# Kernel optimization log

Measured on AMD Instinct MI355X. Metric: run time of the kernel, lower is better.

## Reference

```python
import math
import jax, jax.numpy as jnp
from jax import lax
import numpy as np

B, T, D = 4, 8192, 1024
NUM_PATCHES = 512
EPS = 1e-6

def setup_inputs() -> dict:
    key = jax.random.key(0)
    ks = jax.random.split(key, 4)
    h = D // 2
    x = jax.random.normal(ks[0], (B, T, D), dtype=jnp.float32)
    conv1_w = jax.random.normal(ks[1], (h, D, 3), dtype=jnp.float32) * 0.02
    conv1_b = jnp.zeros((h,), jnp.float32)
    conv2_w = jax.random.normal(ks[2], (1, h, 3), dtype=jnp.float32) * 0.02
    conv2_b = jnp.zeros((1,), jnp.float32)
    norm_w = jnp.ones((D,), jnp.float32)
    return {"x": x, "conv1_w": conv1_w, "conv1_b": conv1_b,
            "conv2_w": conv2_w, "conv2_b": conv2_b, "norm_w": norm_w}

def _conv1d(x_ncw, w, b):
    y = lax.conv_general_dilated(x_ncw, w, window_strides=(1,), padding=[(1, 1)],
                                 dimension_numbers=("NCW", "OIW", "NCW"))
    return y + b[None, :, None]

def reference(x, conv1_w, conv1_b, conv2_w, conv2_b, norm_w):
    b, t, d = x.shape
    k = NUM_PATCHES
    seg = t // k  # T divisible by k, so all segments have equal length

    # LearnedBoundaryPredictor: conv -> gelu -> conv -> logits (B, T)
    xc = jnp.transpose(x, (0, 2, 1))  # (B, D, T)
    hcv = jax.nn.gelu(_conv1d(xc, conv1_w, conv1_b), approximate=False)
    logits = _conv1d(hcv, conv2_w, conv2_b)[:, 0, :]  # (B, T)

    # per-segment softmax-weighted centroid + normalized entropy (vectorized)
    seg_logits = logits.reshape(b, k, seg)
    w = jax.nn.softmax(seg_logits, axis=-1)                      # (B, k, seg)
    pos = jnp.arange(t, dtype=x.dtype).reshape(1, k, seg)
    boundaries = jnp.sum(w * pos, axis=-1)                        # (B, k)
    ent = -jnp.sum(w * jnp.log(jnp.clip(w, 1e-8)), axis=-1)
    entropy_signal = ent / jnp.asarray(math.log(max(seg, 2)), x.dtype)

    # gather byte embeddings at integer boundary positions
    idx = jnp.clip(boundaries.astype(jnp.int32), 0, t - 1)       # (B, k)
    patches = jnp.take_along_axis(x, idx[:, :, None], axis=1)    # (B, k, D)

    # RMSNorm
    rms = lax.rsqrt(jnp.mean(patches * patches, axis=-1, keepdims=True) + EPS)
    out = patches * rms * norm_w
    return out, entropy_signal
```

## Files before the change

### kernel.cpp

```cpp
#include <hip/hip_runtime.h>
#include <hip/hip_bf16.h>
#include <math.h>

#define T_LEN 8192
#define D_DIM 1024
#define H_DIM 512
#define NPATCH 512
#define SEG 16

typedef _Float16 f16;
typedef _Float16 f16x4 __attribute__((ext_vector_type(4)));
typedef _Float16 f16x8 __attribute__((ext_vector_type(8)));
typedef float f32x4 __attribute__((ext_vector_type(4)));

#define BMR 256
#define BNR 128
#define NBM2 128
#define NBN2 4
#define QL2 258
#define PADT (T_LEN + 2)
#define RSCALE 2048.0f
#define RINV   4.8828125e-4f

__device__ __forceinline__ void gll16(const void* g, void* l) {
    __builtin_amdgcn_global_load_lds((const __attribute__((address_space(1))) void*)g,
                                     (__attribute__((address_space(3))) void*)l, 16, 0, 0);
}

__global__ __launch_bounds__(256) void k_split_x(const float* __restrict__ x,
                                                 f16* __restrict__ xh, f16* __restrict__ xls) {
    size_t i4 = (size_t)blockIdx.x * 256 + threadIdx.x;
    size_t e = i4 * 4;
    int d = (int)(e % D_DIM);
    size_t row = e / D_DIM;
    int pt = (int)(row % PADT);
    int b = (int)(row / PADT);
    f16x4 h, lo;
    if (pt == 0 || pt == PADT - 1) {
        h = (f16x4){0, 0, 0, 0}; lo = (f16x4){0, 0, 0, 0};
    } else {
        float4 v = *(const float4*)(x + ((size_t)b * T_LEN + pt - 1) * D_DIM + d);
        f16 h0 = (f16)v.x, h1 = (f16)v.y, h2 = (f16)v.z, h3 = (f16)v.w;
        h = (f16x4){h0, h1, h2, h3};
        lo = (f16x4){(f16)((v.x - (float)h0) * RSCALE), (f16)((v.y - (float)h1) * RSCALE),
                     (f16)((v.z - (float)h2) * RSCALE), (f16)((v.w - (float)h3) * RSCALE)};
    }
    *(f16x4*)(xh + e) = h;
    *(f16x4*)(xls + e) = lo;
}

__global__ void k_split_w(const float* __restrict__ w1, f16* __restrict__ ws) {
    int idx = blockIdx.x * 256 + threadIdx.x;
    if (idx >= 3 * H_DIM * D_DIM) return;
    int i = idx % D_DIM;
    int o = (idx / D_DIM) % H_DIM;
    int j = idx / (D_DIM * H_DIM);
    float v = w1[((size_t)o * D_DIM + i) * 3 + j];
    f16 h = (f16)v;
    f16 l = (f16)((v - (float)h) * RSCALE);
    ws[((size_t)(j * 2 + 0) * H_DIM + o) * D_DIM + i] = h;
    ws[((size_t)(j * 2 + 1) * H_DIM + o) * D_DIM + i] = l;
}

__global__ __launch_bounds__(512, 2) void k_conv_gemm_f16(
    const f16* __restrict__ xh, const f16* __restrict__ xls,
    const f16* __restrict__ wsd, const float* __restrict__ b1,
    const float* __restrict__ w2, float* __restrict__ partials)
{
    __shared__ __align__(16) char smem[55296];
    const int tid = threadIdx.x;
    const int l = tid & 63, wv = tid >> 6;
    const int wr = wv >> 1, wc = wv & 1;

    int bid = blockIdx.x;
    int logical = (bid & 7) * 64 + (bid >> 3);
    const int bm = logical >> 2, bn = logical & 3;
    const int batch = bm >> 5;
    const int lt0 = (bm & 31) * BMR;
    const int n0 = bn * BNR;

    f32x4 ahh[4][4], axx[4][4];
    #pragma unroll
    for (int mi = 0; mi < 4; ++mi)
        #pragma unroll
        for (int nj = 0; nj < 4; ++nj) {
            ahh[mi][nj] = (f32x4){0.f, 0.f, 0.f, 0.f};
            axx[mi][nj] = (f32x4){0.f, 0.f, 0.f, 0.f};
        }

    const int kb = l >> 4, c15 = l & 15;

    for (int j = 0; j < 3; ++j) {
        const f16* ap[6];
        #pragma unroll
        for (int u = 0; u < 6; ++u) {
            int s = wv * 6 + u;
            if (s < 32) {
                int which = s >> 4, sl = s & 15;
                int m = sl * 16 + (l >> 2);
                int ch = (l & 3) ^ ((m >> 1) & 3);
                size_t base = ((size_t)batch * PADT + lt0 + j) * D_DIM;
                ap[u] = (which ? xls : xh) + base + (size_t)m * D_DIM + ch * 8;
            } else {
                int s2 = s - 32, which = s2 >> 3, sl = s2 & 7;
                int n = sl * 16 + (l >> 2);
                int ch = (l & 3) ^ ((n >> 1) & 3);
                size_t base = ((size_t)(j * 2 + which) * H_DIM + n0) * D_DIM;
                ap[u] = wsd + base + (size_t)n * D_DIM + ch * 8;
            }
        }
        for (int k0 = 0; k0 < D_DIM; k0 += 32) {
            #pragma unroll
            for (int u = 0; u < 6; ++u) {
                gll16(ap[u], smem + (wv * 6 + u) * 1024);
                ap[u] += 32;
            }
            __syncthreads();

            f16x8 bh[4], bl[4];
            #pragma unroll
            for (int nj = 0; nj < 4; ++nj) {
                int n = wc * 64 + nj * 16 + c15;
                int boff = n * 64 + ((kb ^ ((n >> 1) & 3)) * 16);
                bh[nj] = *(const f16x8*)(smem + 32768 + boff);
                bl[nj] = *(const f16x8*)(smem + 40960 + boff);
            }
            #pragma unroll
            for (int mi = 0; mi < 4; ++mi) {
                int m = wr * 64 + mi * 16 + c15;
                int aoff = m * 64 + ((kb ^ ((m >> 1) & 3)) * 16);
                f16x8 ah = *(const f16x8*)(smem + aoff);
                f16x8 al = *(const f16x8*)(smem + 16384 + aoff);
                #pragma unroll
                for (int nj = 0; nj < 4; ++nj) {
                    ahh[mi][nj] = __builtin_amdgcn_mfma_f32_16x16x32_f16(ah, bh[nj], ahh[mi][nj], 0, 0, 0);
                    axx[mi][nj] = __builtin_amdgcn_mfma_f32_16x16x32_f16(ah, bl[nj], axx[mi][nj], 0, 0, 0);
                    axx[mi][nj] = __builtin_amdgcn_mfma_f32_16x16x32_f16(al, bh[nj], axx[mi][nj], 0, 0, 0);
                }
            }
            __syncthreads();
        }
    }

    float* lp_lds = (float*)(smem + 49152);
    #pragma unroll
    for (int mi = 0; mi < 4; ++mi) {
        float lp[4][3] = {};
        #pragma unroll
        for (int nj = 0; nj < 4; ++nj) {
            int n = n0 + wc * 64 + nj * 16 + c15;
            float bias = b1[n];
            float w2m1 = w2[n * 3 + 2];
            float w20  = w2[n * 3 + 1];
            float w2p1 = w2[n * 3 + 0];
            #pragma unroll
            for (int r = 0; r < 4; ++r) {
                float v = ahh[mi][nj][r] + axx[mi][nj][r] * RINV + bias;
                float g = 0.5f * v * (1.f + erff(v * 0.70710678118654752f));
                lp[r][0] = fmaf(g, w2m1, lp[r][0]);
                lp[r][1] = fmaf(g, w20,  lp[r][1]);
                lp[r][2] = fmaf(g, w2p1, lp[r][2]);
            }
        }
        #pragma unroll
        for (int r = 0; r < 4; ++r)
            #pragma unroll
            for (int d = 0; d < 3; ++d) {
                float v = lp[r][d];
                v += __shfl_xor(v, 1, 64);
                v += __shfl_xor(v, 2, 64);
                v += __shfl_xor(v, 4, 64);
                v += __shfl_xor(v, 8, 64);
                lp[r][d] = v;
            }
        if (c15 == 0) {
            int m = wr * 64 + mi * 16 + kb * 4;
            #pragma unroll
            for (int r = 0; r < 4; ++r)
                #pragma unroll
                for (int d = 0; d < 3; ++d)
                    lp_lds[(wc * 3 + d) * 256 + m + r] = lp[r][d];
        }
    }
    __syncthreads();

    float* pout = partials + (size_t)(bm * NBN2 + bn) * QL2;
    for (int q = tid; q < QL2; q += 512) {
        int tloc = lt0 + q - 1;
        if (tloc >= 0 && tloc < T_LEN) {
            float v = 0.f;
            #pragma unroll
            for (int w2c = 0; w2c < 2; ++w2c) {
                if (q >= 1 && q <= 256) v += lp_lds[(w2c * 3 + 1) * 256 + q - 1];
                if (q >= 2)             v += lp_lds[(w2c * 3 + 2) * 256 + q - 2];
                if (q < 256)            v += lp_lds[(w2c * 3 + 0) * 256 + q];
            }
            pout[q] = v;
        }
    }
}

__global__ void k_reduce2(const float* __restrict__ partials,
                          const float* __restrict__ b2, float* __restrict__ logits) {
    int M = blockIdx.x * 256 + threadIdx.x;
    if (M >= 4 * T_LEN) return;
    int t = M & (T_LEN - 1);
    int bm = M >> 8;
    int mq = M & 255;
    int q = mq + 1;
    float s = b2[0];
    #pragma unroll
    for (int bn = 0; bn < NBN2; ++bn)
        s += partials[(size_t)(bm * NBN2 + bn) * QL2 + q];
    if (mq == 0 && t != 0) {
        #pragma unroll
        for (int bn = 0; bn < NBN2; ++bn)
            s += partials[(size_t)((bm - 1) * NBN2 + bn) * QL2 + (QL2 - 1)];
    }
    if (mq == 255 && t != T_LEN - 1) {
        #pragma unroll
        for (int bn = 0; bn < NBN2; ++bn)
            s += partials[(size_t)((bm + 1) * NBN2 + bn) * QL2 + 0];
    }
    logits[M] = s;
}

__global__ __launch_bounds__(256) void k_finalize(
    const float* __restrict__ x, const float* __restrict__ logits,
    const float* __restrict__ norm_w, float* __restrict__ out)
{
    int blk = blockIdx.x;
    int b = blk >> 9, p = blk & 511;
    const float* lg = logits + b * T_LEN + p * SEG;

    float l[SEG];
    #pragma unroll
    for (int i = 0; i < SEG; ++i) l[i] = lg[i];
    float mx = l[0];
    #pragma unroll
    for (int i = 1; i < SEG; ++i) mx = fmaxf(mx, l[i]);
    float w[SEG];
    float s = 0.f;
    #pragma unroll
    for (int i = 0; i < SEG; ++i) { w[i] = expf(l[i] - mx); s += w[i]; }
    float inv = 1.f / s;
    float boundary = 0.f, ent = 0.f;
    #pragma unroll
    for (int i = 0; i < SEG; ++i) {
        float wi = w[i] * inv;
        boundary += wi * (float)(p * SEG + i);
        ent -= wi * logf(fmaxf(wi, 1e-8f));
    }
    ent *= 0.36067376022224085f;

    int idx = (int)boundary;
    idx = min(max(idx, 0), T_LEN - 1);

    const float* row = x + ((size_t)b * T_LEN + idx) * D_DIM;
    int tid = threadIdx.x;
    float v[4];
    float ss = 0.f;
    #pragma unroll
    for (int r = 0; r < 4; ++r) {
        int c = tid + r * 256;
        v[r] = row[c];
        ss = fmaf(v[r], v[r], ss);
    }
    #pragma unroll
    for (int off = 32; off > 0; off >>= 1) ss += __shfl_down(ss, off, 64);
    __shared__ float sred[4];
    if ((tid & 63) == 0) sred[tid >> 6] = ss;
    __syncthreads();
    float tot = sred[0] + sred[1] + sred[2] + sred[3];
    float rms = rsqrtf(tot * (1.f / 1024.f) + 1e-6f);

    float* o0 = out + ((size_t)b * NPATCH + p) * D_DIM;
    #pragma unroll
    for (int r = 0; r < 4; ++r) {
        int c = tid + r * 256;
        o0[c] = v[r] * rms * norm_w[c];
    }
    if (tid == 0)
        out[(size_t)4 * NPATCH * D_DIM + b * NPATCH + p] = ent;
}

#define BM 128
#define BN 128
#define BK 16
#define NBM (4 * T_LEN / BM)
#define NBN (H_DIM / BN)
#define QLEN 130

__global__ void k_transpose_w1(const float* __restrict__ w1, float* __restrict__ w1t) {
    int idx = blockIdx.x * 256 + threadIdx.x;
    if (idx >= 3 * D_DIM * H_DIM) return;
    int o = idx % H_DIM;
    int i = (idx / H_DIM) % D_DIM;
    int j = idx / (H_DIM * D_DIM);
    w1t[idx] = w1[(o * D_DIM + i) * 3 + j];
}

__global__ __launch_bounds__(256) void k_conv_gemm(
    const float* __restrict__ x, const float* __restrict__ w1t,
    const float* __restrict__ b1, const float* __restrict__ w2,
    float* __restrict__ partials)
{
    __shared__ float As[BK][BM + 4];
    __shared__ float Bs[BK][BN];
    __shared__ float ld_lp[3][BM];

    const int bm = blockIdx.x, bn = blockIdx.y;
    const int m0 = bm * BM;
    const int batch = m0 / T_LEN;
    const int t0 = m0 % T_LEN;
    const int n0 = bn * BN;
    const int tid = threadIdx.x;
    const int tx = tid & 15, ty = tid >> 4;

    float acc[8][8] = {};

    const int a_col = (tid & 3) * 4;
    const int a_row = tid >> 2;
    const int b_row = tid >> 5;
    const int b_col = (tid & 31) * 4;

    const float* xb = x + (size_t)batch * T_LEN * D_DIM;

    for (int j = 0; j < 3; ++j) {
        const float* wj = w1t + (size_t)j * D_DIM * H_DIM;
        const int tshift = j - 1;
        for (int k0 = 0; k0 < D_DIM; k0 += BK) {
            #pragma unroll
            for (int rr = 0; rr < 2; ++rr) {
                int m = a_row + rr * 64;
                int tt = t0 + m + tshift;
                float4 v = make_float4(0.f, 0.f, 0.f, 0.f);
                if (tt >= 0 && tt < T_LEN)
                    v = *(const float4*)(xb + (size_t)tt * D_DIM + k0 + a_col);
                As[a_col + 0][m] = v.x; As[a_col + 1][m] = v.y;
                As[a_col + 2][m] = v.z; As[a_col + 3][m] = v.w;
            }
            #pragma unroll
            for (int rr = 0; rr < 2; ++rr) {
                int kk = b_row + rr * 8;
                *(float4*)&Bs[kk][b_col] =
                    *(const float4*)(wj + (size_t)(k0 + kk) * H_DIM + n0 + b_col);
            }
            __syncthreads();
            #pragma unroll
            for (int kk = 0; kk < BK; ++kk) {
                float a[8], bb[8];
                *(float4*)&a[0]  = *(const float4*)&As[kk][ty * 8];
                *(float4*)&a[4]  = *(const float4*)&As[kk][ty * 8 + 4];
                *(float4*)&bb[0] = *(const float4*)&Bs[kk][tx * 8];
                *(float4*)&bb[4] = *(const float4*)&Bs[kk][tx * 8 + 4];
                #pragma unroll
                for (int i = 0; i < 8; ++i) {
                    #pragma unroll
                    for (int ll = 0; ll < 8; ++ll)
                        acc[i][ll] = fmaf(a[i], bb[ll], acc[i][ll]);
                }
            }
            __syncthreads();
        }
    }

    float lp[8][3];
    #pragma unroll
    for (int i = 0; i < 8; ++i) { lp[i][0] = 0.f; lp[i][1] = 0.f; lp[i][2] = 0.f; }
    #pragma unroll
    for (int ll = 0; ll < 8; ++ll) {
        int n = n0 + tx * 8 + ll;
        float bias = b1[n];
        float w2m1 = w2[n * 3 + 2];
        float w20  = w2[n * 3 + 1];
        float w2p1 = w2[n * 3 + 0];
        #pragma unroll
        for (int i = 0; i < 8; ++i) {
            float v = acc[i][ll] + bias;
            float g = 0.5f * v * (1.f + erff(v * 0.70710678118654752f));
            lp[i][0] = fmaf(g, w2m1, lp[i][0]);
            lp[i][1] = fmaf(g, w20,  lp[i][1]);
            lp[i][2] = fmaf(g, w2p1, lp[i][2]);
        }
    }
    #pragma unroll
    for (int i = 0; i < 8; ++i) {
        #pragma unroll
        for (int d = 0; d < 3; ++d) {
            float v = lp[i][d];
            v += __shfl_xor(v, 1, 64);
            v += __shfl_xor(v, 2, 64);
            v += __shfl_xor(v, 4, 64);
            v += __shfl_xor(v, 8, 64);
            lp[i][d] = v;
        }
    }
    if (tx == 0) {
        #pragma unroll
        for (int i = 0; i < 8; ++i) {
            ld_lp[0][ty * 8 + i] = lp[i][0];
            ld_lp[1][ty * 8 + i] = lp[i][1];
            ld_lp[2][ty * 8 + i] = lp[i][2];
        }
    }
    __syncthreads();
    float* pout = partials + (size_t)(bm * NBN + bn) * QLEN;
    for (int q = tid; q < QLEN; q += 256) {
        int t = t0 + q - 1;
        if (t >= 0 && t < T_LEN) {
            float v = 0.f;
            if (q >= 1 && q <= BM) v += ld_lp[1][q - 1];
            if (q >= 2)            v += ld_lp[2][q - 2];
            if (q < BM)            v += ld_lp[0][q];
            pout[q] = v;
        }
    }
}

__global__ void k_reduce_logits(const float* __restrict__ partials,
                                const float* __restrict__ b2,
                                float* __restrict__ logits) {
    int M = blockIdx.x * 256 + threadIdx.x;
    if (M >= 4 * T_LEN) return;
    int t = M % T_LEN;
    int bm = M / BM;
    int q = (M % BM) + 1;
    float s = b2[0];
    #pragma unroll
    for (int bn = 0; bn < NBN; ++bn)
        s += partials[(size_t)(bm * NBN + bn) * QLEN + q];
    if ((M % BM) == 0 && t != 0) {
        #pragma unroll
        for (int bn = 0; bn < NBN; ++bn)
            s += partials[(size_t)((bm - 1) * NBN + bn) * QLEN + (QLEN - 1)];
    }
    if ((M % BM) == BM - 1 && t != T_LEN - 1) {
        #pragma unroll
        for (int bn = 0; bn < NBN; ++bn)
            s += partials[(size_t)((bm + 1) * NBN + bn) * QLEN + 0];
    }
    logits[M] = s;
}

extern "C" void kernel_launch(void* const* d_in, const int* in_sizes, int n_in,
                              void* d_out, int out_size, void* d_ws, size_t ws_size,
                              hipStream_t stream) {
    const float* x  = (const float*)d_in[0];
    const float* w1 = (const float*)d_in[1];
    const float* b1 = (const float*)d_in[2];
    const float* w2 = (const float*)d_in[3];
    const float* b2 = (const float*)d_in[4];
    const float* nw = (const float*)d_in[5];
    float* out = (float*)d_out;

    const size_t XS_ELEMS = (size_t)4 * PADT * D_DIM;
    const size_t WS_ELEMS = (size_t)3 * 2 * H_DIM * D_DIM;
    const size_t P2_FLOATS = (size_t)NBM2 * NBN2 * QL2;
    const size_t NEED = XS_ELEMS * 2 * sizeof(f16) + WS_ELEMS * sizeof(f16)
                      + (P2_FLOATS + 4 * T_LEN) * sizeof(float);

    if (ws_size >= NEED) {
        f16* xh = (f16*)d_ws;
        f16* xls = xh + XS_ELEMS;
        f16* wsd = xls + XS_ELEMS;
        float* partials = (float*)(wsd + WS_ELEMS);
        float* logits = partials + P2_FLOATS;

        k_split_x<<<(int)(XS_ELEMS / 4 / 256), 256, 0, stream>>>(x, xh, xls);
        k_split_w<<<(3 * H_DIM * D_DIM + 255) / 256, 256, 0, stream>>>(w1, wsd);
        k_conv_gemm_f16<<<NBM2 * NBN2, 512, 0, stream>>>(xh, xls, wsd, b1, w2, partials);
        k_reduce2<<<(4 * T_LEN + 255) / 256, 256, 0, stream>>>(partials, b2, logits);
        k_finalize<<<2048, 256, 0, stream>>>(x, logits, nw, out);
    } else {
        float* w1t      = (float*)d_ws;
        float* partials = w1t + 3 * D_DIM * H_DIM;
        float* logits   = partials + (size_t)NBM * NBN * QLEN;

        k_transpose_w1<<<(3 * D_DIM * H_DIM + 255) / 256, 256, 0, stream>>>(w1, w1t);
        k_conv_gemm<<<dim3(NBM, NBN), 256, 0, stream>>>(x, w1t, b1, w2, partials);
        k_reduce_logits<<<(4 * T_LEN + 255) / 256, 256, 0, stream>>>(partials, b2, logits);
        k_finalize<<<2048, 256, 0, stream>>>(x, logits, nw, out);
    }
}
```

Before: 405.6 us.

## Triple-buffer conv GEMM LDS staging with interleaved async loads and MFMA phases

Replaces the single-buffered, two-barrier k-loop in the conv GEMM with a flattened 96-step loop over a triple-buffered LDS ring, prefetching two steps ahead via global_load_lds. Loads for the next stages are issued in pairs between MFMA quadrants, and the MFMA blocks are wrapped in s_setprio to favour compute issue. The aim is to hide global-memory latency behind the MFMAs. In exchange, LDS use grows to about 150KB per block, which may cut the two blocks per CU that launch_bounds targets, and the loop adds more barriers.

```diff
diff --git a/kernel.cpp b/kernel.cpp
--- a/kernel.cpp
+++ b/kernel.cpp
@@ -21,6 +21,9 @@
 #define PADT (T_LEN + 2)
 #define RSCALE 2048.0f
 #define RINV   4.8828125e-4f
+
+#define BUFB 49152
+#define NSTEP 96
 
 __device__ __forceinline__ void gll16(const void* g, void* l) {
     __builtin_amdgcn_global_load_lds((const __attribute__((address_space(1))) void*)g,
@@ -62,12 +65,26 @@
     ws[((size_t)(j * 2 + 1) * H_DIM + o) * D_DIM + i] = l;
 }
 
+#define MM3(mi, nj, AH, AL, BH, BL)                                                       \
+    ahh[mi][nj] = __builtin_amdgcn_mfma_f32_16x16x32_f16(AH, BH, ahh[mi][nj], 0, 0, 0);   \
+    axx[mi][nj] = __builtin_amdgcn_mfma_f32_16x16x32_f16(AH, BL, axx[mi][nj], 0, 0, 0);   \
+    axx[mi][nj] = __builtin_amdgcn_mfma_f32_16x16x32_f16(AL, BH, axx[mi][nj], 0, 0, 0);
+
+#define STAGE_PAIR(SV, U0, U1)                                                            \
+    { int sv_ = (SV);                                                                     \
+      if (sv_ < NSTEP) {                                                                  \
+          char* dsty = smem + (sv_ % 3) * BUFB;                                           \
+          int jj_ = sv_ >> 5; int ko_ = (sv_ & 31) * 32;                                  \
+          gll16(base0[U0] + (size_t)jj_ * jstr[U0] + ko_, dsty + (wv * 6 + U0) * 1024);   \
+          gll16(base0[U1] + (size_t)jj_ * jstr[U1] + ko_, dsty + (wv * 6 + U1) * 1024);   \
+      } }
+
 __global__ __launch_bounds__(512, 2) void k_conv_gemm_f16(
     const f16* __restrict__ xh, const f16* __restrict__ xls,
     const f16* __restrict__ wsd, const float* __restrict__ b1,
     const float* __restrict__ w2, float* __restrict__ partials)
 {
-    __shared__ __align__(16) char smem[55296];
+    __shared__ __align__(16) char smem[3 * BUFB + 6144];
     const int tid = threadIdx.x;
     const int l = tid & 63, wv = tid >> 6;
     const int wr = wv >> 1, wc = wv & 1;
@@ -90,59 +107,97 @@
 
     const int kb = l >> 4, c15 = l & 15;
 
-    for (int j = 0; j < 3; ++j) {
-        const f16* ap[6];
-        #pragma unroll
-        for (int u = 0; u < 6; ++u) {
-            int s = wv * 6 + u;
-            if (s < 32) {
-                int which = s >> 4, sl = s & 15;
-                int m = sl * 16 + (l >> 2);
-                int ch = (l & 3) ^ ((m >> 1) & 3);
-                size_t base = ((size_t)batch * PADT + lt0 + j) * D_DIM;
-                ap[u] = (which ? xls : xh) + base + (size_t)m * D_DIM + ch * 8;
-            } else {
-                int s2 = s - 32, which = s2 >> 3, sl = s2 & 7;
-                int n = sl * 16 + (l >> 2);
-                int ch = (l & 3) ^ ((n >> 1) & 3);
-                size_t base = ((size_t)(j * 2 + which) * H_DIM + n0) * D_DIM;
-                ap[u] = wsd + base + (size_t)n * D_DIM + ch * 8;
-            }
-        }
-        for (int k0 = 0; k0 < D_DIM; k0 += 32) {
-            #pragma unroll
-            for (int u = 0; u < 6; ++u) {
-                gll16(ap[u], smem + (wv * 6 + u) * 1024);
-                ap[u] += 32;
-            }
-            __syncthreads();
-
-            f16x8 bh[4], bl[4];
-            #pragma unroll
-            for (int nj = 0; nj < 4; ++nj) {
-                int n = wc * 64 + nj * 16 + c15;
-                int boff = n * 64 + ((kb ^ ((n >> 1) & 3)) * 16);
-                bh[nj] = *(const f16x8*)(smem + 32768 + boff);
-                bl[nj] = *(const f16x8*)(smem + 40960 + boff);
-            }
-            #pragma unroll
-            for (int mi = 0; mi < 4; ++mi) {
-                int m = wr * 64 + mi * 16 + c15;
-                int aoff = m * 64 + ((kb ^ ((m >> 1) & 3)) * 16);
-                f16x8 ah = *(const f16x8*)(smem + aoff);
-                f16x8 al = *(const f16x8*)(smem + 16384 + aoff);
-                #pragma unroll
-                for (int nj = 0; nj < 4; ++nj) {
-                    ahh[mi][nj] = __builtin_amdgcn_mfma_f32_16x16x32_f16(ah, bh[nj], ahh[mi][nj], 0, 0, 0);
-                    axx[mi][nj] = __builtin_amdgcn_mfma_f32_16x16x32_f16(ah, bl[nj], axx[mi][nj], 0, 0, 0);
-                    axx[mi][nj] = __builtin_amdgcn_mfma_f32_16x16x32_f16(al, bh[nj], axx[mi][nj], 0, 0, 0);
-                }
-            }
-            __syncthreads();
-        }
-    }
-
-    float* lp_lds = (float*)(smem + 49152);
+    const f16* base0[6];
+    int jstr[6];
+    #pragma unroll
+    for (int u = 0; u < 6; ++u) {
+        int s = wv * 6 + u;
+        if (s < 32) {
+            int which = s >> 4, sl = s & 15;
+            int m = sl * 16 + (l >> 2);
+            int ch = (l & 3) ^ ((m >> 1) & 3);
+            base0[u] = (which ? xls : xh) + ((size_t)batch * PADT + lt0) * D_DIM
+                       + (size_t)m * D_DIM + ch * 8;
+            jstr[u] = D_DIM;
+        } else {
+            int s2 = s - 32, which = s2 >> 3, sl = s2 & 7;
+            int n = sl * 16 + (l >> 2);
+            int ch = (l & 3) ^ ((n >> 1) & 3);
+            base0[u] = wsd + ((size_t)which * H_DIM + n0) * D_DIM + (size_t)n * D_DIM + ch * 8;
+            jstr[u] = 2 * H_DIM * D_DIM;
+        }
+    }
+
+    int aoff_[4], boff_[4];
+    #pragma unroll
+    for (int mi = 0; mi < 4; ++mi) {
+        int m = wr * 64 + mi * 16 + c15;
+        aoff_[mi] = m * 64 + ((kb ^ ((m >> 1) & 3)) * 16);
+    }
+    #pragma unroll
+    for (int nj = 0; nj < 4; ++nj) {
+        int n = wc * 64 + nj * 16 + c15;
+        boff_[nj] = n * 64 + ((kb ^ ((n >> 1) & 3)) * 16);
+    }
+
+    #pragma unroll
+    for (int u = 0; u < 6; ++u)
+        gll16(base0[u], smem + (wv * 6 + u) * 1024);
+    #pragma unroll
+    for (int u = 0; u < 6; ++u)
+        gll16(base0[u] + 32, smem + BUFB + (wv * 6 + u) * 1024);
+    asm volatile("s_waitcnt vmcnt(6)" ::: "memory");
+    __builtin_amdgcn_s_barrier();
+
+    for (int t = 0; t < NSTEP; ++t) {
+        char* buf = smem + (t % 3) * BUFB;
+        f16x8 ah0, al0, ah1, al1, ah2, al2, ah3, al3;
+        f16x8 bh0, bl0, bh1, bl1, bh2, bl2, bh3, bl3;
+
+        ah0 = *(const f16x8*)(buf + aoff_[0]);          al0 = *(const f16x8*)(buf + 16384 + aoff_[0]);
+        ah1 = *(const f16x8*)(buf + aoff_[1]);          al1 = *(const f16x8*)(buf + 16384 + aoff_[1]);
+        bh0 = *(const f16x8*)(buf + 32768 + boff_[0]);  bl0 = *(const f16x8*)(buf + 40960 + boff_[0]);
+        bh1 = *(const f16x8*)(buf + 32768 + boff_[1]);  bl1 = *(const f16x8*)(buf + 40960 + boff_[1]);
+        STAGE_PAIR(t + 2, 0, 1);
+        __builtin_amdgcn_s_barrier();
+        __builtin_amdgcn_s_setprio(1);
+        MM3(0, 0, ah0, al0, bh0, bl0); MM3(0, 1, ah0, al0, bh1, bl1);
+        MM3(1, 0, ah1, al1, bh0, bl0); MM3(1, 1, ah1, al1, bh1, bl1);
+        __builtin_amdgcn_s_setprio(0);
+        __builtin_amdgcn_s_barrier();
+
+        ah2 = *(const f16x8*)(buf + aoff_[2]);          al2 = *(const f16x8*)(buf + 16384 + aoff_[2]);
+        ah3 = *(const f16x8*)(buf + aoff_[3]);          al3 = *(const f16x8*)(buf + 16384 + aoff_[3]);
+        STAGE_PAIR(t + 2, 2, 3);
+        __builtin_amdgcn_s_barrier();
+        __builtin_amdgcn_s_setprio(1);
+        MM3(2, 0, ah2, al2, bh0, bl0); MM3(2, 1, ah2, al2, bh1, bl1);
+        MM3(3, 0, ah3, al3, bh0, bl0); MM3(3, 1, ah3, al3, bh1, bl1);
+        __builtin_amdgcn_s_setprio(0);
+        __builtin_amdgcn_s_barrier();
+
+        bh2 = *(const f16x8*)(buf + 32768 + boff_[2]);  bl2 = *(const f16x8*)(buf + 40960 + boff_[2]);
+        bh3 = *(const f16x8*)(buf + 32768 + boff_[3]);  bl3 = *(const f16x8*)(buf + 40960 + boff_[3]);
+        STAGE_PAIR(t + 2, 4, 5);
+        __builtin_amdgcn_s_barrier();
+        __builtin_amdgcn_s_setprio(1);
+        MM3(2, 2, ah2, al2, bh2, bl2); MM3(2, 3, ah2, al2, bh3, bl3);
+        MM3(3, 2, ah3, al3, bh2, bl2); MM3(3, 3, ah3, al3, bh3, bl3);
+        __builtin_amdgcn_s_setprio(0);
+        __builtin_amdgcn_s_barrier();
+
+        __builtin_amdgcn_s_setprio(1);
+        MM3(0, 2, ah0, al0, bh2, bl2); MM3(0, 3, ah0, al0, bh3, bl3);
+        MM3(1, 2, ah1, al1, bh2, bl2); MM3(1, 3, ah1, al1, bh3, bl3);
+        __builtin_amdgcn_s_setprio(0);
+        if (t < NSTEP - 2)
+            asm volatile("s_waitcnt vmcnt(6)" ::: "memory");
+        else if (t == NSTEP - 2)
+            asm volatile("s_waitcnt vmcnt(0)" ::: "memory");
+        __builtin_amdgcn_s_barrier();
+    }
+
+    float* lp_lds = (float*)(smem + 3 * BUFB);
     #pragma unroll
     for (int mi = 0; mi < 4; ++mi) {
         float lp[4][3] = {};
```

Measured after the change: 357.1 us. 1.14x faster.

## Double-buffer LDS in conv GEMM with smaller 128x128 tiles and fused tap loop

Applied to the files above, without the earlier changes.

Rewrites the f16 split-precision conv GEMM to use 128x128 tiles with 256 threads and 1024 blocks. The three conv taps are merged into one 96-step K loop, and LDS is double-buffered so the next global-to-LDS load overlaps the current MFMAs, with one barrier per step and raised wave priority during the MFMAs. The old dedicated reduce kernel is dropped in favour of the existing k_reduce_logits with matching partial sizes. The cost is smaller tiles, which means more redundant A/B traffic per output, and the code depends on NBM/NBN/QLEN matching the new 128-row tiling.

```diff
diff --git a/kernel.cpp b/kernel.cpp
--- a/kernel.cpp
+++ b/kernel.cpp
@@ -13,14 +13,11 @@
 typedef _Float16 f16x8 __attribute__((ext_vector_type(8)));
 typedef float f32x4 __attribute__((ext_vector_type(4)));
 
-#define BMR 256
-#define BNR 128
-#define NBM2 128
-#define NBN2 4
-#define QL2 258
 #define PADT (T_LEN + 2)
 #define RSCALE 2048.0f
 #define RINV   4.8828125e-4f
+#define NSTEP 96
+#define BUF2B 32768
 
 __device__ __forceinline__ void gll16(const void* g, void* l) {
     __builtin_amdgcn_global_load_lds((const __attribute__((address_space(1))) void*)g,
@@ -62,22 +59,69 @@
     ws[((size_t)(j * 2 + 1) * H_DIM + o) * D_DIM + i] = l;
 }
 
-__global__ __launch_bounds__(512, 2) void k_conv_gemm_f16(
+#define MM3(mi, nj, AH, AL, BH, BL)                                                       \
+    ahh[mi][nj] = __builtin_amdgcn_mfma_f32_16x16x32_f16(AH, BH, ahh[mi][nj], 0, 0, 0);   \
+    axx[mi][nj] = __builtin_amdgcn_mfma_f32_16x16x32_f16(AH, BL, axx[mi][nj], 0, 0, 0);   \
+    axx[mi][nj] = __builtin_amdgcn_mfma_f32_16x16x32_f16(AL, BH, axx[mi][nj], 0, 0, 0);
+
+#define STEP(T_, RB_, DB_)                                                                \
+{                                                                                         \
+    const int t_ = (T_);                                                                  \
+    char* buf = (RB_);                                                                    \
+             \
+    if (t_ + 1 < NSTEP) {                                                                 \
+        char* dsty = (DB_);                                                               \
+        _Pragma("unroll")                                                                 \
+        for (int u = 0; u < 8; ++u)                                                       \
+            gll16(ap[u], dsty + (wv * 8 + u) * 1024);                                     \
+    }                                                                                     \
+    {                                                                                     \
+        bool bnd = (((t_ + 1) & 31) == 31);                                               \
+        _Pragma("unroll")                                                                 \
+        for (int u = 0; u < 8; ++u)                                                       \
+            ap[u] += bnd ? (jstr[u] - 992) : 32;                                          \
+    }                                                                                     \
+    f16x8 ah0, al0, ah1, al1, ah2, al2, ah3, al3;                                         \
+    f16x8 bh0, bl0, bh1, bl1, bh2, bl2, bh3, bl3;                                         \
+    ah0 = *(const f16x8*)(buf + aoff_[0]);          al0 = *(const f16x8*)(buf + 8192 + aoff_[0]);   \
+    ah1 = *(const f16x8*)(buf + aoff_[1]);          al1 = *(const f16x8*)(buf + 8192 + aoff_[1]);   \
+    ah2 = *(const f16x8*)(buf + aoff_[2]);          al2 = *(const f16x8*)(buf + 8192 + aoff_[2]);   \
+    ah3 = *(const f16x8*)(buf + aoff_[3]);          al3 = *(const f16x8*)(buf + 8192 + aoff_[3]);   \
+    bh0 = *(const f16x8*)(buf + 16384 + boff_[0]);  bl0 = *(const f16x8*)(buf + 24576 + boff_[0]);  \
+    bh1 = *(const f16x8*)(buf + 16384 + boff_[1]);  bl1 = *(const f16x8*)(buf + 24576 + boff_[1]);  \
+    bh2 = *(const f16x8*)(buf + 16384 + boff_[2]);  bl2 = *(const f16x8*)(buf + 24576 + boff_[2]);  \
+    bh3 = *(const f16x8*)(buf + 16384 + boff_[3]);  bl3 = *(const f16x8*)(buf + 24576 + boff_[3]);  \
+    __builtin_amdgcn_s_setprio(1);                                                        \
+    MM3(0, 0, ah0, al0, bh0, bl0); MM3(0, 1, ah0, al0, bh1, bl1);                         \
+    MM3(1, 0, ah1, al1, bh0, bl0); MM3(1, 1, ah1, al1, bh1, bl1);                         \
+    MM3(2, 0, ah2, al2, bh0, bl0); MM3(2, 1, ah2, al2, bh1, bl1);                         \
+    MM3(3, 0, ah3, al3, bh0, bl0); MM3(3, 1, ah3, al3, bh1, bl1);                         \
+    MM3(2, 2, ah2, al2, bh2, bl2); MM3(2, 3, ah2, al2, bh3, bl3);                         \
+    MM3(3, 2, ah3, al3, bh2, bl2); MM3(3, 3, ah3, al3, bh3, bl3);                         \
+    MM3(0, 2, ah0, al0, bh2, bl2); MM3(0, 3, ah0, al0, bh3, bl3);                         \
+    MM3(1, 2, ah1, al1, bh2, bl2); MM3(1, 3, ah1, al1, bh3, bl3);                         \
+    __builtin_amdgcn_s_setprio(0);                                                        \
+    if (t_ < NSTEP - 1)                                                                   \
+        asm volatile("s_waitcnt vmcnt(0)" ::: "memory");                                  \
+    __builtin_amdgcn_s_barrier();                                                         \
+}
+
+__global__ __launch_bounds__(256, 2) void k_conv_gemm_f16(
     const f16* __restrict__ xh, const f16* __restrict__ xls,
     const f16* __restrict__ wsd, const float* __restrict__ b1,
     const float* __restrict__ w2, float* __restrict__ partials)
 {
-    __shared__ __align__(16) char smem[55296];
+    __shared__ __align__(16) char smem[2 * BUF2B + 3072];
     const int tid = threadIdx.x;
     const int l = tid & 63, wv = tid >> 6;
     const int wr = wv >> 1, wc = wv & 1;
 
     int bid = blockIdx.x;
-    int logical = (bid & 7) * 64 + (bid >> 3);
+    int logical = (bid & 7) * 128 + (bid >> 3);
     const int bm = logical >> 2, bn = logical & 3;
-    const int batch = bm >> 5;
-    const int lt0 = (bm & 31) * BMR;
-    const int n0 = bn * BNR;
+    const int batch = bm >> 6;
+    const int lt0 = (bm & 63) * 128;
+    const int n0 = bn * 128;
 
     f32x4 ahh[4][4], axx[4][4];
     #pragma unroll
@@ -90,59 +134,55 @@
 
     const int kb = l >> 4, c15 = l & 15;
 
-    for (int j = 0; j < 3; ++j) {
-        const f16* ap[6];
-        #pragma unroll
-        for (int u = 0; u < 6; ++u) {
-            int s = wv * 6 + u;
-            if (s < 32) {
-                int which = s >> 4, sl = s & 15;
-                int m = sl * 16 + (l >> 2);
-                int ch = (l & 3) ^ ((m >> 1) & 3);
-                size_t base = ((size_t)batch * PADT + lt0 + j) * D_DIM;
-                ap[u] = (which ? xls : xh) + base + (size_t)m * D_DIM + ch * 8;
-            } else {
-                int s2 = s - 32, which = s2 >> 3, sl = s2 & 7;
-                int n = sl * 16 + (l >> 2);
-                int ch = (l & 3) ^ ((n >> 1) & 3);
-                size_t base = ((size_t)(j * 2 + which) * H_DIM + n0) * D_DIM;
-                ap[u] = wsd + base + (size_t)n * D_DIM + ch * 8;
-            }
-        }
-        for (int k0 = 0; k0 < D_DIM; k0 += 32) {
-            #pragma unroll
-            for (int u = 0; u < 6; ++u) {
-                gll16(ap[u], smem + (wv * 6 + u) * 1024);
-                ap[u] += 32;
-            }
-            __syncthreads();
-
-            f16x8 bh[4], bl[4];
-            #pragma unroll
-            for (int nj = 0; nj < 4; ++nj) {
-                int n = wc * 64 + nj * 16 + c15;
-                int boff = n * 64 + ((kb ^ ((n >> 1) & 3)) * 16);
-                bh[nj] = *(const f16x8*)(smem + 32768 + boff);
-                bl[nj] = *(const f16x8*)(smem + 40960 + boff);
-            }
-            #pragma unroll
-            for (int mi = 0; mi < 4; ++mi) {
-                int m = wr * 64 + mi * 16 + c15;
-                int aoff = m * 64 + ((kb ^ ((m >> 1) & 3)) * 16);
-                f16x8 ah = *(const f16x8*)(smem + aoff);
-                f16x8 al = *(const f16x8*)(smem + 16384 + aoff);
-                #pragma unroll
-                for (int nj = 0; nj < 4; ++nj) {
-                    ahh[mi][nj] = __builtin_amdgcn_mfma_f32_16x16x32_f16(ah, bh[nj], ahh[mi][nj], 0, 0, 0);
-                    axx[mi][nj] = __builtin_amdgcn_mfma_f32_16x16x32_f16(ah, bl[nj], axx[mi][nj], 0, 0, 0);
-                    axx[mi][nj] = __builtin_amdgcn_mfma_f32_16x16x32_f16(al, bh[nj], axx[mi][nj], 0, 0, 0);
-                }
-            }
-            __syncthreads();
-        }
-    }
-
-    float* lp_lds = (float*)(smem + 49152);
+    const f16* base0[8];
+    int jstr[8];
+    #pragma unroll
+    for (int u = 0; u < 8; ++u) {
+        int S = wv * 8 + u;
+        int sl = S & 7;
+        int m = sl * 16 + (l >> 2);
+        int ch = (l & 3) ^ ((m >> 1) & 3);
+        if (S < 16) {
+            const f16* src = (S < 8) ? xh : xls;
+            base0[u] = src + ((size_t)batch * PADT + lt0) * D_DIM + (size_t)m * D_DIM + ch * 8;
+            jstr[u] = D_DIM;
+        } else {
+            int which = (S >= 24);
+            base0[u] = wsd + ((size_t)which * H_DIM + n0) * D_DIM + (size_t)m * D_DIM + ch * 8;
+            jstr[u] = 2 * H_DIM * D_DIM;
+        }
+    }
+
+    int aoff_[4], boff_[4];
+    #pragma unroll
+    for (int mi = 0; mi < 4; ++mi) {
+        int m = wr * 64 + mi * 16 + c15;
+        aoff_[mi] = m * 64 + ((kb ^ ((m >> 1) & 3)) * 16);
+    }
+    #pragma unroll
+    for (int nj = 0; nj < 4; ++nj) {
+        int n = wc * 64 + nj * 16 + c15;
+        boff_[nj] = n * 64 + ((kb ^ ((n >> 1) & 3)) * 16);
+    }
+
+    char* B0 = smem;
+    char* B1 = smem + BUF2B;
+
+    const f16* ap[8];
+    #pragma unroll
+    for (int u = 0; u < 8; ++u) {
+        gll16(base0[u], B0 + (wv * 8 + u) * 1024);
+        ap[u] = base0[u] + 32;
+    }
+    asm volatile("s_waitcnt vmcnt(0)" ::: "memory");
+    __builtin_amdgcn_s_barrier();
+
+    for (int tt = 0; tt < NSTEP; tt += 2) {
+        STEP(tt,     B0, B1);
+        STEP(tt + 1, B1, B0);
+    }
+
+    float* lp_lds = (float*)(smem + 2 * BUF2B);
     #pragma unroll
     for (int mi = 0; mi < 4; ++mi) {
         float lp[4][3] = {};
@@ -179,50 +219,25 @@
             for (int r = 0; r < 4; ++r)
                 #pragma unroll
                 for (int d = 0; d < 3; ++d)
-                    lp_lds[(wc * 3 + d) * 256 + m + r] = lp[r][d];
+                    lp_lds[(wc * 3 + d) * 128 + m + r] = lp[r][d];
         }
     }
     __syncthreads();
 
-    float* pout = partials + (size_t)(bm * NBN2 + bn) * QL2;
-    for (int q = tid; q < QL2; q += 512) {
+    float* pout = partials + (size_t)(bm * 4 + bn) * 130;
+    for (int q = tid; q < 130; q += 256) {
         int tloc = lt0 + q - 1;
         if (tloc >= 0 && tloc < T_LEN) {
             float v = 0.f;
             #pragma unroll
             for (int w2c = 0; w2c < 2; ++w2c) {
-                if (q >= 1 && q <= 256) v += lp_lds[(w2c * 3 + 1) * 256 + q - 1];
-                if (q >= 2)             v += lp_lds[(w2c * 3 + 2) * 256 + q - 2];
-                if (q < 256)            v += lp_lds[(w2c * 3 + 0) * 256 + q];
+                if (q >= 1 && q <= 128) v += lp_lds[(w2c * 3 + 1) * 128 + q - 1];
+                if (q >= 2)             v += lp_lds[(w2c * 3 + 2) * 128 + q - 2];
+                if (q < 128)            v += lp_lds[(w2c * 3 + 0) * 128 + q];
             }
             pout[q] = v;
         }
     }
-}
-
-__global__ void k_reduce2(const float* __restrict__ partials,
-                          const float* __restrict__ b2, float* __restrict__ logits) {
-    int M = blockIdx.x * 256 + threadIdx.x;
-    if (M >= 4 * T_LEN) return;
-    int t = M & (T_LEN - 1);
-    int bm = M >> 8;
-    int mq = M & 255;
-    int q = mq + 1;
-    float s = b2[0];
-    #pragma unroll
-    for (int bn = 0; bn < NBN2; ++bn)
-        s += partials[(size_t)(bm * NBN2 + bn) * QL2 + q];
-    if (mq == 0 && t != 0) {
-        #pragma unroll
-        for (int bn = 0; bn < NBN2; ++bn)
-            s += partials[(size_t)((bm - 1) * NBN2 + bn) * QL2 + (QL2 - 1)];
-    }
-    if (mq == 255 && t != T_LEN - 1) {
-        #pragma unroll
-        for (int bn = 0; bn < NBN2; ++bn)
-            s += partials[(size_t)((bm + 1) * NBN2 + bn) * QL2 + 0];
-    }
-    logits[M] = s;
 }
 
 __global__ __launch_bounds__(256) void k_finalize(
@@ -456,21 +471,21 @@
 
     const size_t XS_ELEMS = (size_t)4 * PADT * D_DIM;
     const size_t WS_ELEMS = (size_t)3 * 2 * H_DIM * D_DIM;
-    const size_t P2_FLOATS = (size_t)NBM2 * NBN2 * QL2;
+    const size_t P_FLOATS = (size_t)NBM * NBN * QLEN;
     const size_t NEED = XS_ELEMS * 2 * sizeof(f16) + WS_ELEMS * sizeof(f16)
-                      + (P2_FLOATS + 4 * T_LEN) * sizeof(float);
+                      + (P_FLOATS + 4 * T_LEN) * sizeof(float);
 
     if (ws_size >= NEED) {
         f16* xh = (f16*)d_ws;
         f16* xls = xh + XS_ELEMS;
         f16* wsd = xls + XS_ELEMS;
         float* partials = (float*)(wsd + WS_ELEMS);
-        float* logits = partials + P2_FLOATS;
+        float* logits = partials + P_FLOATS;
 
         k_split_x<<<(int)(XS_ELEMS / 4 / 256), 256, 0, stream>>>(x, xh, xls);
         k_split_w<<<(3 * H_DIM * D_DIM + 255) / 256, 256, 0, stream>>>(w1, wsd);
-        k_conv_gemm_f16<<<NBM2 * NBN2, 512, 0, stream>>>(xh, xls, wsd, b1, w2, partials);
-        k_reduce2<<<(4 * T_LEN + 255) / 256, 256, 0, stream>>>(partials, b2, logits);
+        k_conv_gemm_f16<<<1024, 256, 0, stream>>>(xh, xls, wsd, b1, w2, partials);
+        k_reduce_logits<<<(4 * T_LEN + 255) / 256, 256, 0, stream>>>(partials, b2, logits);
         k_finalize<<<2048, 256, 0, stream>>>(x, logits, nw, out);
     } else {
         float* w1t      = (float*)d_ws;
```

Result: faster. 349.1 us (-13.9%).

## Triple-buffer A tile in LDS and stream B fragments directly from global

Applied to the files above, without the earlier changes.

Restructures the conv GEMM main loop into a 96-step software pipeline. The A tiles (x hi/lo) are triple-buffered in LDS and loaded asynchronously. The weight B fragments skip LDS and are loaded straight into registers from global memory, double-buffered one step ahead. This replaces the two __syncthreads per k-step with one barrier plus explicit vmcnt waits, and raises MFMA priority with s_setprio. The three conv taps are merged into one continuous k-loop by shifting the A row and jumping the B offset, which removes the per-tap reload setup. In exchange it uses more registers, LDS and hand-tuned waitcnt counts that must match the number of loads in flight.

```diff
diff --git a/kernel.cpp b/kernel.cpp
--- a/kernel.cpp
+++ b/kernel.cpp
@@ -21,6 +21,10 @@
 #define PADT (T_LEN + 2)
 #define RSCALE 2048.0f
 #define RINV   4.8828125e-4f
+
+#define ABUFB 32768
+#define NSTEP 96
+#define BJUMP ((uint32_t)(2 * H_DIM * D_DIM - 992) * 2)
 
 __device__ __forceinline__ void gll16(const void* g, void* l) {
     __builtin_amdgcn_global_load_lds((const __attribute__((address_space(1))) void*)g,
@@ -62,12 +66,61 @@
     ws[((size_t)(j * 2 + 1) * H_DIM + o) * D_DIM + i] = l;
 }
 
+#define MM3(mi, nj, AH, AL, BH, BL)                                                       \
+    ahh[mi][nj] = __builtin_amdgcn_mfma_f32_16x16x32_f16(AH, BH, ahh[mi][nj], 0, 0, 0);   \
+    axx[mi][nj] = __builtin_amdgcn_mfma_f32_16x16x32_f16(AH, BL, axx[mi][nj], 0, 0, 0);   \
+    axx[mi][nj] = __builtin_amdgcn_mfma_f32_16x16x32_f16(AL, BH, axx[mi][nj], 0, 0, 0);
+
+#define LOADB(BH_, BL_)                                                                   \
+    { _Pragma("unroll")                                                                   \
+      for (int q = 0; q < 4; ++q) BH_[q] = *(const f16x8*)((const char*)wsd + boff[q]);   \
+      _Pragma("unroll")                                                                   \
+      for (int q = 0; q < 4; ++q) BL_[q] = *(const f16x8*)((const char*)wsd + boff[4+q]); }
+
+#define ADVB(SNEXT_)                                                                      \
+    { uint32_t d_ = ((((SNEXT_)) & 31) == 0) ? BJUMP : 64u;                               \
+      _Pragma("unroll")                                                                   \
+      for (int q = 0; q < 8; ++q) boff[q] += d_; }
+
+#define GBODY(T_, ABUF_, DBUF_, BCH_, BCL_, BNH_, BNL_, DOB_, DOA_)                       \
+{                                                                                         \
+    if (DOB_) { LOADB(BNH_, BNL_); ADVB((T_) + 2); }                                      \
+    if (DOA_) {                                                                           \
+        char* dsty_ = (DBUF_);                                                            \
+        _Pragma("unroll")                                                                 \
+        for (int u = 0; u < 4; ++u) {                                                     \
+            gll16((const char*)abase + aoffg[u], dsty_ + (wv * 4 + u) * 1024);            \
+            aoffg[u] += 64;                                                               \
+        }                                                                                 \
+    }                                                                                     \
+    char* buf_ = (ABUF_);                                                                 \
+    f16x8 ah0, al0, ah1, al1, ah2, al2, ah3, al3;                                         \
+    ah0 = *(const f16x8*)(buf_ + aoff_[0]);  al0 = *(const f16x8*)(buf_ + 16384 + aoff_[0]); \
+    ah1 = *(const f16x8*)(buf_ + aoff_[1]);  al1 = *(const f16x8*)(buf_ + 16384 + aoff_[1]); \
+    ah2 = *(const f16x8*)(buf_ + aoff_[2]);  al2 = *(const f16x8*)(buf_ + 16384 + aoff_[2]); \
+    ah3 = *(const f16x8*)(buf_ + aoff_[3]);  al3 = *(const f16x8*)(buf_ + 16384 + aoff_[3]); \
+    __builtin_amdgcn_s_setprio(1);                                                        \
+    MM3(0, 0, ah0, al0, BCH_[0], BCL_[0]); MM3(0, 1, ah0, al0, BCH_[1], BCL_[1]);         \
+    MM3(1, 0, ah1, al1, BCH_[0], BCL_[0]); MM3(1, 1, ah1, al1, BCH_[1], BCL_[1]);         \
+    MM3(2, 0, ah2, al2, BCH_[0], BCL_[0]); MM3(2, 1, ah2, al2, BCH_[1], BCL_[1]);         \
+    MM3(3, 0, ah3, al3, BCH_[0], BCL_[0]); MM3(3, 1, ah3, al3, BCH_[1], BCL_[1]);         \
+    MM3(2, 2, ah2, al2, BCH_[2], BCL_[2]); MM3(2, 3, ah2, al2, BCH_[3], BCL_[3]);         \
+    MM3(3, 2, ah3, al3, BCH_[2], BCL_[2]); MM3(3, 3, ah3, al3, BCH_[3], BCL_[3]);         \
+    MM3(0, 2, ah0, al0, BCH_[2], BCL_[2]); MM3(0, 3, ah0, al0, BCH_[3], BCL_[3]);         \
+    MM3(1, 2, ah1, al1, BCH_[2], BCL_[2]); MM3(1, 3, ah1, al1, BCH_[3], BCL_[3]);         \
+    __builtin_amdgcn_s_setprio(0);                                                        \
+}
+
+#define WAIT12 asm volatile("s_waitcnt vmcnt(12)" ::: "memory")
+#define WAIT8  asm volatile("s_waitcnt vmcnt(8)"  ::: "memory")
+#define BAR    __builtin_amdgcn_s_barrier()
+
 __global__ __launch_bounds__(512, 2) void k_conv_gemm_f16(
     const f16* __restrict__ xh, const f16* __restrict__ xls,
     const f16* __restrict__ wsd, const float* __restrict__ b1,
     const float* __restrict__ w2, float* __restrict__ partials)
 {
-    __shared__ __align__(16) char smem[55296];
+    __shared__ __align__(16) char smem[3 * ABUFB + 6144];
     const int tid = threadIdx.x;
     const int l = tid & 63, wv = tid >> 6;
     const int wr = wv >> 1, wc = wv & 1;
@@ -90,59 +143,68 @@
 
     const int kb = l >> 4, c15 = l & 15;
 
-    for (int j = 0; j < 3; ++j) {
-        const f16* ap[6];
-        #pragma unroll
-        for (int u = 0; u < 6; ++u) {
-            int s = wv * 6 + u;
-            if (s < 32) {
-                int which = s >> 4, sl = s & 15;
-                int m = sl * 16 + (l >> 2);
-                int ch = (l & 3) ^ ((m >> 1) & 3);
-                size_t base = ((size_t)batch * PADT + lt0 + j) * D_DIM;
-                ap[u] = (which ? xls : xh) + base + (size_t)m * D_DIM + ch * 8;
-            } else {
-                int s2 = s - 32, which = s2 >> 3, sl = s2 & 7;
-                int n = sl * 16 + (l >> 2);
-                int ch = (l & 3) ^ ((n >> 1) & 3);
-                size_t base = ((size_t)(j * 2 + which) * H_DIM + n0) * D_DIM;
-                ap[u] = wsd + base + (size_t)n * D_DIM + ch * 8;
-            }
-        }
-        for (int k0 = 0; k0 < D_DIM; k0 += 32) {
-            #pragma unroll
-            for (int u = 0; u < 6; ++u) {
-                gll16(ap[u], smem + (wv * 6 + u) * 1024);
-                ap[u] += 32;
-            }
-            __syncthreads();
-
-            f16x8 bh[4], bl[4];
-            #pragma unroll
-            for (int nj = 0; nj < 4; ++nj) {
-                int n = wc * 64 + nj * 16 + c15;
-                int boff = n * 64 + ((kb ^ ((n >> 1) & 3)) * 16);
-                bh[nj] = *(const f16x8*)(smem + 32768 + boff);
-                bl[nj] = *(const f16x8*)(smem + 40960 + boff);
-            }
-            #pragma unroll
-            for (int mi = 0; mi < 4; ++mi) {
-                int m = wr * 64 + mi * 16 + c15;
-                int aoff = m * 64 + ((kb ^ ((m >> 1) & 3)) * 16);
-                f16x8 ah = *(const f16x8*)(smem + aoff);
-                f16x8 al = *(const f16x8*)(smem + 16384 + aoff);
-                #pragma unroll
-                for (int nj = 0; nj < 4; ++nj) {
-                    ahh[mi][nj] = __builtin_amdgcn_mfma_f32_16x16x32_f16(ah, bh[nj], ahh[mi][nj], 0, 0, 0);
-                    axx[mi][nj] = __builtin_amdgcn_mfma_f32_16x16x32_f16(ah, bl[nj], axx[mi][nj], 0, 0, 0);
-                    axx[mi][nj] = __builtin_amdgcn_mfma_f32_16x16x32_f16(al, bh[nj], axx[mi][nj], 0, 0, 0);
-                }
-            }
-            __syncthreads();
-        }
-    }
-
-    float* lp_lds = (float*)(smem + 49152);
+    const f16* abase = (wv < 4) ? xh : xls;
+    uint32_t aoffg[4];
+    #pragma unroll
+    for (int u = 0; u < 4; ++u) {
+        int S = wv * 4 + u;
+        int sl = S & 15;
+        int m = sl * 16 + (l >> 2);
+        int ch = (l & 3) ^ ((m >> 1) & 3);
+        aoffg[u] = (uint32_t)(((((uint32_t)batch * PADT + lt0 + m) * D_DIM) + ch * 8) * 2);
+    }
+
+    uint32_t boff[8];
+    #pragma unroll
+    for (int p = 0; p < 2; ++p)
+        #pragma unroll
+        for (int nj = 0; nj < 4; ++nj) {
+            int n = n0 + wc * 64 + nj * 16 + c15;
+            boff[p * 4 + nj] = (uint32_t)(((((uint32_t)p * H_DIM + n) * D_DIM) + kb * 8) * 2);
+        }
+
+    int aoff_[4];
+    #pragma unroll
+    for (int mi = 0; mi < 4; ++mi) {
+        int m = wr * 64 + mi * 16 + c15;
+        aoff_[mi] = m * 64 + ((kb ^ ((m >> 1) & 3)) * 16);
+    }
+
+    char* A0 = smem;
+    char* A1 = smem + ABUFB;
+    char* A2 = smem + 2 * ABUFB;
+
+    f16x8 bAh[4], bAl[4], bBh[4], bBl[4];
+
+    #pragma unroll
+    for (int u = 0; u < 4; ++u)
+        gll16((const char*)abase + aoffg[u], A0 + (wv * 4 + u) * 1024);
+    #pragma unroll
+    for (int u = 0; u < 4; ++u) {
+        gll16((const char*)abase + aoffg[u] + 64, A1 + (wv * 4 + u) * 1024);
+        aoffg[u] += 128;
+    }
+    LOADB(bAh, bAl);
+    ADVB(1);
+    WAIT12;
+    BAR;
+
+    for (int tt = 0; tt < 90; tt += 6) {
+        GBODY(tt + 0, A0, A2, bAh, bAl, bBh, bBl, 1, 1); WAIT12; BAR;
+        GBODY(tt + 1, A1, A0, bBh, bBl, bAh, bAl, 1, 1); WAIT12; BAR;
+        GBODY(tt + 2, A2, A1, bAh, bAl, bBh, bBl, 1, 1); WAIT12; BAR;
+        GBODY(tt + 3, A0, A2, bBh, bBl, bAh, bAl, 1, 1); WAIT12; BAR;
+        GBODY(tt + 4, A1, A0, bAh, bAl, bBh, bBl, 1, 1); WAIT12; BAR;
+        GBODY(tt + 5, A2, A1, bBh, bBl, bAh, bAl, 1, 1); WAIT12; BAR;
+    }
+    GBODY(90, A0, A2, bAh, bAl, bBh, bBl, 1, 1); WAIT12; BAR;
+    GBODY(91, A1, A0, bBh, bBl, bAh, bAl, 1, 1); WAIT12; BAR;
+    GBODY(92, A2, A1, bAh, bAl, bBh, bBl, 1, 1); WAIT12; BAR;
+    GBODY(93, A0, A2, bBh, bBl, bAh, bAl, 1, 1); WAIT12; BAR;
+    GBODY(94, A1, A0, bAh, bAl, bBh, bBl, 1, 0); WAIT8;  BAR;
+    GBODY(95, A2, A1, bBh, bBl, bAh, bAl, 0, 0);         BAR;
+
+    float* lp_lds = (float*)(smem + 3 * ABUFB);
     #pragma unroll
     for (int mi = 0; mi < 4; ++mi) {
         float lp[4][3] = {};
```

Result: slower. 824.5 us (+103.3%).
